# Kernel tuning notes

Hardware: AMD Instinct MI355X
Metric: run time of the kernel (lower is better)

## Reference

```python
import jax, jax.numpy as jnp
import numpy as np

EPS = 1e-5
HEADS = 8


def _bn(x, p):
    # p: [4, C] rows = (gamma, beta, running_mean, running_var); channel axis = 1 (eval-mode BN)
    shape = (1, p.shape[1]) + (1,) * (x.ndim - 2)
    g = p[0].reshape(shape); b = p[1].reshape(shape)
    m = p[2].reshape(shape); v = p[3].reshape(shape)
    return (x - m) * (g / jnp.sqrt(v + EPS)) + b


def _conv1x1(x, w):
    # x: [N, Cin, H, W], w: [Cout, Cin]
    return jnp.einsum('oc,nchw->nohw', w, x)


def _axial(x, kqv_w, kqv_bn, logits_bn, rel_enc, ks, height_dim):
    # x: [B, C, H, W]
    if height_dim:
        x = jnp.transpose(x, (0, 3, 1, 2))  # [B, W, C, H] -> attend over H (=ks)
    else:
        x = jnp.transpose(x, (0, 2, 1, 3))  # [B, H, C, W] -> attend over W (=ks)
    b, w, d, h = x.shape
    dh = d // HEADS
    xf = x.reshape(b * w, d, h)
    kqv = jnp.einsum('oc,ncl->nol', kqv_w, xf)          # conv1d k=1, [n, 2d, h]
    kqv = _bn(kqv, kqv_bn)
    kqv = kqv.reshape(b * w, HEADS, dh * 2, h)
    k = kqv[:, :, : dh // 2]                            # [n, H, dh/2, h]
    q = kqv[:, :, dh // 2: dh]                          # [n, H, dh/2, h]
    v = kqv[:, :, dh:]                                  # [n, H, dh,   h]
    # relative position encodings
    idx = jnp.arange(ks)[None, :] - jnp.arange(ks)[:, None] + ks - 1  # [ks, ks]
    rel = rel_enc[:, idx.reshape(-1)].reshape(dh * 2, ks, ks)
    q_enc = rel[: dh // 2]
    k_enc = rel[dh // 2: dh]
    v_enc = rel[dh:]
    qk = jnp.einsum('nhdx,nhdy->nhxy', q, k)
    qr = jnp.einsum('nhdx,dxy->nhxy', q, q_enc)
    kr = jnp.einsum('nhdx,dxy->nhyx', k, k_enc)         # einsum + transpose(2,3)
    logits = jnp.concatenate([qk, qr, kr], axis=1)       # [n, 3*H, h, h]
    logits = _bn(logits, logits_bn)
    logits = logits.reshape(b * w, 3, HEADS, h, h).sum(axis=1)
    weights = jax.nn.softmax(logits, axis=3)             # [n, H, h, h]
    attn = jnp.einsum('nhxy,nhdy->nhdx', weights, v)
    attn_enc = jnp.einsum('nhxy,dxy->nhdx', weights, v_enc)
    # cat along last dim + reshape + sum(dim=-2) in torch == elementwise sum here
    out = (attn + attn_enc).reshape(b, w, d, h)
    if height_dim:
        out = jnp.transpose(out, (0, 2, 3, 1))  # [B, C, H, W]
    else:
        out = jnp.transpose(out, (0, 2, 1, 3))  # [B, C, H, W]
    return out


def setup_inputs() -> dict:
    key = jax.random.key(0)
    ks = jax.random.split(key, 13)
    def rn(k, shape, s=0.05):
        return jax.random.normal(k, shape, jnp.float32) * s
    def rp(k, shape):
        return jax.random.uniform(k, shape, jnp.float32, minval=0.1, maxval=1.0)
    return {
        'x': jax.random.normal(ks[0], (1, 64, 256, 128), jnp.float32),
        'conv1_w': rn(ks[1], (64, 64)),
        'bn1': rp(ks[2], (4, 64)),
        'kqv_w_h': rn(ks[3], (128, 64)),
        'kqv_bn_h': rp(ks[4], (4, 128)),
        'logits_bn_h': rp(ks[5], (4, 24)),
        'rel_enc_h': rn(ks[6], (16, 511)),
        'kqv_w_w': rn(ks[7], (128, 64)),
        'kqv_bn_w': rp(ks[8], (4, 128)),
        'logits_bn_w': rp(ks[9], (4, 24)),
        'rel_enc_w': rn(ks[10], (16, 255)),
        'conv3_w': rn(ks[11], (64, 64)),
        'bn3': rp(ks[12], (4, 64)),
    }


def reference(x, conv1_w, bn1, kqv_w_h, kqv_bn_h, logits_bn_h, rel_enc_h,
              kqv_w_w, kqv_bn_w, logits_bn_w, rel_enc_w, conv3_w, bn3):
    out = jax.nn.relu(_bn(_conv1x1(x, conv1_w), bn1))
    out = _axial(out, kqv_w_h, kqv_bn_h, logits_bn_h, rel_enc_h, 256, True)
    out = _axial(out, kqv_w_w, kqv_bn_w, logits_bn_w, rel_enc_w, 128, False)
    out = jax.nn.relu(out)
    out = _bn(_conv1x1(out, conv3_w), bn3)
    return jax.nn.relu(out + x)
```

## Files before the change

### kernel.cpp

```cpp
#include <hip/hip_runtime.h>
#include <stdint.h>

#define EPSF 1e-5f
#define LOG2E 1.4426950408889634f

__device__ __forceinline__ float bflo(uint32_t u){ union{uint32_t u;float f;}c; c.u=u<<16; return c.f; }
__device__ __forceinline__ float bfhi(uint32_t u){ union{uint32_t u;float f;}c; c.u=u&0xffff0000u; return c.f; }
__device__ __forceinline__ float bfhiraw(uint32_t u){ union{uint32_t u;float f;}c; c.u=u; return c.f; }
__device__ __forceinline__ uint32_t f2bf(float f){ union{float f;uint32_t u;}c; c.f=f; uint32_t u=c.u; return (u + 0x7fffu + ((u>>16)&1u)) >> 16; }
__device__ __forceinline__ uint32_t pk2(float a, float b){ return f2bf(a) | (f2bf(b)<<16); }

__global__ void k_relpack(const float* __restrict__ relH, const float* __restrict__ relW,
                          uint4* __restrict__ rqkH, uint4* __restrict__ rveH,
                          uint4* __restrict__ rqkW, uint4* __restrict__ rveW) {
  int NJ = blockIdx.x ? 255 : 511;
  const float* rel = blockIdx.x ? relW : relH;
  uint4* rqk = blockIdx.x ? rqkW : rqkH;
  uint4* rve = blockIdx.x ? rveW : rveH;
  int j = threadIdx.x;
  if (j >= NJ) return;
  const float* q = rel;
  const float* k = rel + 4*NJ;
  const float* v = rel + 8*NJ;
  int jr = NJ-1-j;
  uint4 a;
  a.x = pk2(q[0*NJ+j], q[1*NJ+j]);
  a.y = pk2(q[2*NJ+j], q[3*NJ+j]);
  a.z = pk2(k[0*NJ+jr], k[1*NJ+jr]);
  a.w = pk2(k[2*NJ+jr], k[3*NJ+jr]);
  rqk[j] = a;
  uint4 b;
  b.x = pk2(v[0*NJ+j], v[1*NJ+j]);
  b.y = pk2(v[2*NJ+j], v[3*NJ+j]);
  b.z = pk2(v[4*NJ+j], v[5*NJ+j]);
  b.w = pk2(v[6*NJ+j], v[7*NJ+j]);
  rve[j] = b;
}

__global__ __launch_bounds__(256)
void k_conv1(const float* __restrict__ in, const float* __restrict__ w,
             const float* __restrict__ bn, float* __restrict__ out) {
  __shared__ float L[64*65];
  int tid = threadIdx.x;
  int p0 = blockIdx.x * 64;
  int lane = tid & 63;
  int wvs = __builtin_amdgcn_readfirstlane(tid >> 6);
  #pragma unroll
  for (int rr = 0; rr < 16; ++rr) {
    int c = wvs*16 + rr;
    L[c*64 + lane] = in[(size_t)c*32768 + p0 + lane];
  }
  __syncthreads();
  float xv[64];
  #pragma unroll
  for (int c = 0; c < 64; ++c) xv[c] = L[c*64 + lane];
  float val[16];
  #pragma unroll
  for (int r = 0; r < 16; ++r) {
    int o = wvs*16 + r;
    const float* wr = w + o*64;
    float acc = 0.f;
    #pragma unroll
    for (int c = 0; c < 64; ++c) acc = fmaf(wr[c], xv[c], acc);
    float s = bn[o] * rsqrtf(bn[192+o] + EPSF);
    val[r] = fmaxf(fmaf(acc, s, fmaf(-bn[128+o], s, bn[64+o])), 0.f);
  }
  __syncthreads();
  #pragma unroll
  for (int r = 0; r < 16; ++r) L[lane*65 + wvs*16 + r] = val[r];
  __syncthreads();
  float4* dst = (float4*)(out + (size_t)p0*64);
  #pragma unroll
  for (int k = 0; k < 4; ++k) {
    int f4 = tid + k*256;
    int f = f4*4; int p = f >> 6, o = f & 63;
    float4 v;
    v.x = L[p*65+o]; v.y = L[p*65+o+1]; v.z = L[p*65+o+2]; v.w = L[p*65+o+3];
    dst[f4] = v;
  }
}

template<int LEN, int RS, int CS>
__global__ __launch_bounds__(512)
void k_kqv(const float* __restrict__ in, const float* __restrict__ w,
           const float* __restrict__ bn, uint4* __restrict__ kvV,
           uint2* __restrict__ kvK, float* __restrict__ qb) {
  __shared__ float L[64*65];
  int tid = threadIdx.x;
  int n = blockIdx.x;
  int y0 = blockIdx.y * 64;
  #pragma unroll
  for (int rr = 0; rr < 8; ++rr) {
    int idx = tid + rr*512;
    int yy = idx >> 6, c = idx & 63;
    L[yy*65 + c] = in[((size_t)(y0+yy)*RS + (size_t)n*CS)*64 + c];
  }
  __syncthreads();
  int hd = __builtin_amdgcn_readfirstlane(tid >> 6);
  int yy = tid & 63;
  float xv[64];
  #pragma unroll
  for (int c = 0; c < 64; ++c) xv[c] = L[yy*65 + c];
  float val[16];
  #pragma unroll
  for (int r = 0; r < 16; ++r) {
    int o = hd*16 + r;
    const float* wr = w + o*64;
    float acc = 0.f;
    #pragma unroll
    for (int c = 0; c < 64; ++c) acc = fmaf(wr[c], xv[c], acc);
    float s = bn[o] * rsqrtf(bn[384+o] + EPSF);
    val[r] = fmaf(acc, s, fmaf(-bn[256+o], s, bn[128+o]));
  }
  size_t base = ((size_t)n*8 + hd)*LEN + (y0 + yy);
  kvK[base] = make_uint2(pk2(val[0],val[1]), pk2(val[2],val[3]));
  kvV[base] = make_uint4(pk2(val[8],val[9]),  pk2(val[10],val[11]),
                         pk2(val[12],val[13]), pk2(val[14],val[15]));
  float4 qq; qq.x = val[4]; qq.y = val[5]; qq.z = val[6]; qq.w = val[7];
  *(float4*)(qb + base*4) = qq;
}

template<int LEN, int G, bool RELUO, int XS, int NS>
__global__ __launch_bounds__(LEN*G/2, 2)
void k_attn2(const uint4* __restrict__ kvV, const uint2* __restrict__ kvK,
             const float* __restrict__ qb, const uint4* __restrict__ rqk,
             const uint4* __restrict__ rve, const float* __restrict__ lbn,
             float* __restrict__ out) {
  constexpr int NJ = 2*LEN-1;
  constexpr int HALF = LEN/2;
  constexpr int T = LEN*G/2;
  constexpr int YR = LEN/G;
  constexpr int CH = 4;
  constexpr size_t S1 = (size_t)LEN*48 + (size_t)NJ*48;
  constexpr size_t S2 = (size_t)(G-1)*LEN*40;
  constexpr size_t PS = S1 > S2 ? S1 : S2;
  int n  = blockIdx.x >> 3;
  int hd = blockIdx.x & 7;
  int t  = threadIdx.x;

  __shared__ __align__(16) char pool[PS];
  float4* sK   = (float4*)(pool);
  float4* sVa  = (float4*)(pool + (size_t)LEN*16);
  float4* sVb  = (float4*)(pool + (size_t)LEN*32);
  uint4*  sT   = (uint4*) (pool + (size_t)LEN*48);
  float4* sVE0 = (float4*)(pool + (size_t)LEN*48 + (size_t)NJ*16);
  float4* sVE1 = (float4*)(pool + (size_t)LEN*48 + (size_t)NJ*32);

  size_t kvbase = ((size_t)n*8 + hd)*LEN;
  for (int i = t; i < LEN; i += T) {
    uint2 kk = kvK[kvbase + i];
    uint4 vv = kvV[kvbase + i];
    sK[i]  = make_float4(bflo(kk.x), bfhi(kk.x), bflo(kk.y), bfhi(kk.y));
    sVa[i] = make_float4(bflo(vv.x), bfhi(vv.x), bflo(vv.y), bfhi(vv.y));
    sVb[i] = make_float4(bflo(vv.z), bfhi(vv.z), bflo(vv.w), bfhi(vv.w));
  }
  for (int j = t; j < NJ; j += T) {
    sT[j] = rqk[j];
    uint4 ve = rve[j];
    sVE0[j] = make_float4(bflo(ve.x), bfhi(ve.x), bflo(ve.y), bfhi(ve.y));
    sVE1[j] = make_float4(bflo(ve.z), bfhi(ve.z), bflo(ve.w), bfhi(ve.w));
  }

  float A0,A1,A2,Bc;
  {
    int c0 = hd, c1 = 8+hd, c2 = 16+hd;
    float s0 = lbn[c0]*rsqrtf(lbn[72+c0]+EPSF);
    float s1 = lbn[c1]*rsqrtf(lbn[72+c1]+EPSF);
    float s2 = lbn[c2]*rsqrtf(lbn[72+c2]+EPSF);
    float t0 = fmaf(-lbn[48+c0], s0, lbn[24+c0]);
    float t1 = fmaf(-lbn[48+c1], s1, lbn[24+c1]);
    float t2 = fmaf(-lbn[48+c2], s2, lbn[24+c2]);
    A0 = s0*LOG2E; A1 = s1*LOG2E; A2 = s2*LOG2E; Bc = (t0+t1+t2)*LOG2E;
  }

  int g  = t / HALF;
  int tl = t % HALF;
  int y0 = g * YR;

  float q[2][4];
  #pragma unroll
  for (int i = 0; i < 2; ++i) {
    float4 qq = *(const float4*)(qb + (kvbase + tl + i*HALF)*4);
    q[i][0]=qq.x; q[i][1]=qq.y; q[i][2]=qq.z; q[i][3]=qq.w;
  }
  float m[2], ss[2], acc[2][8], lr[2][CH];
  #pragma unroll
  for (int i=0;i<2;++i){ m[i]=-3.0e38f; ss[i]=0.f;
    #pragma unroll
    for(int d=0;d<8;++d) acc[i][d]=0.f; }

  __syncthreads();

  for (int yc = 0; yc < YR; yc += CH) {
    #pragma unroll
    for (int c = 0; c < CH; ++c) {
      int y = y0 + yc + c;
      float4 kk = sK[y];
      #pragma unroll
      for (int i = 0; i < 2; ++i) {
        int j = y - (tl + i*HALF) + (LEN-1);
        uint4 qe = sT[j];
        float qk = fmaf(q[i][3],kk.w, fmaf(q[i][2],kk.z, fmaf(q[i][1],kk.y, q[i][0]*kk.x)));
        float qr = fmaf(q[i][1],bfhiraw(qe.x), q[i][0]*bflo(qe.x));
        qr = fmaf(q[i][3],bfhiraw(qe.y), fmaf(q[i][2],bflo(qe.y), qr));
        float kr = fmaf(kk.y,bfhiraw(qe.z), kk.x*bflo(qe.z));
        kr = fmaf(kk.w,bfhiraw(qe.w), fmaf(kk.z,bflo(qe.w), kr));
        lr[i][c] = fmaf(qk,A0, fmaf(qr,A1, fmaf(kr,A2, Bc)));
      }
    }
    #pragma unroll
    for (int i = 0; i < 2; ++i) {
      float cm = fmaxf(fmaxf(lr[i][0], lr[i][1]), fmaxf(lr[i][2], lr[i][3]));
      float mn = fmaxf(m[i], cm);
      float sc = __builtin_amdgcn_exp2f(m[i] - mn);
      m[i] = mn; ss[i] *= sc;
      #pragma unroll
      for (int d = 0; d < 8; ++d) acc[i][d] *= sc;
    }
    #pragma unroll
    for (int c = 0; c < CH; ++c) {
      int y = y0 + yc + c;
      float4 va = sVa[y], vb = sVb[y];
      #pragma unroll
      for (int i = 0; i < 2; ++i) {
        int j = y - (tl + i*HALF) + (LEN-1);
        float4 ea = sVE0[j];
        float4 eb = sVE1[j];
        float e = __builtin_amdgcn_exp2f(lr[i][c] - m[i]);
        ss[i] += e;
        acc[i][0] = fmaf(e, va.x + ea.x, acc[i][0]);
        acc[i][1] = fmaf(e, va.y + ea.y, acc[i][1]);
        acc[i][2] = fmaf(e, va.z + ea.z, acc[i][2]);
        acc[i][3] = fmaf(e, va.w + ea.w, acc[i][3]);
        acc[i][4] = fmaf(e, vb.x + eb.x, acc[i][4]);
        acc[i][5] = fmaf(e, vb.y + eb.y, acc[i][5]);
        acc[i][6] = fmaf(e, vb.z + eb.z, acc[i][6]);
        acc[i][7] = fmaf(e, vb.w + eb.w, acc[i][7]);
      }
    }
  }

  __syncthreads();
  float4* M0 = (float4*)(pool);
  float4* M1 = (float4*)(pool + (size_t)(G-1)*LEN*16);
  float2* MS = (float2*)(pool + (size_t)(G-1)*LEN*32);
  if (g > 0) {
    #pragma unroll
    for (int i = 0; i < 2; ++i) {
      int slot = ((g-1)*HALF + tl)*2 + i;
      M0[slot] = make_float4(acc[i][0],acc[i][1],acc[i][2],acc[i][3]);
      M1[slot] = make_float4(acc[i][4],acc[i][5],acc[i][6],acc[i][7]);
      MS[slot] = make_float2(m[i], ss[i]);
    }
  }
  __syncthreads();
  if (g == 0) {
    #pragma unroll
    for (int i = 0; i < 2; ++i) {
      float M = m[i];
      float2 oms[G-1];
      #pragma unroll
      for (int gg = 1; gg < G; ++gg) {
        oms[gg-1] = MS[((gg-1)*HALF + tl)*2 + i];
        M = fmaxf(M, oms[gg-1].x);
      }
      float w0 = __builtin_amdgcn_exp2f(m[i] - M);
      float st = ss[i]*w0;
      float a[8];
      #pragma unroll
      for (int d = 0; d < 8; ++d) a[d] = acc[i][d]*w0;
      #pragma unroll
      for (int gg = 1; gg < G; ++gg) {
        int slot = ((gg-1)*HALF + tl)*2 + i;
        float wg = __builtin_amdgcn_exp2f(oms[gg-1].x - M);
        st += oms[gg-1].y*wg;
        float4 a0 = M0[slot];
        float4 a1 = M1[slot];
        a[0] = fmaf(a0.x, wg, a[0]); a[1] = fmaf(a0.y, wg, a[1]);
        a[2] = fmaf(a0.z, wg, a[2]); a[3] = fmaf(a0.w, wg, a[3]);
        a[4] = fmaf(a1.x, wg, a[4]); a[5] = fmaf(a1.y, wg, a[5]);
        a[6] = fmaf(a1.z, wg, a[6]); a[7] = fmaf(a1.w, wg, a[7]);
      }
      float inv = 1.0f / st;
      int x = tl + i*HALF;
      float* dst = out + ((size_t)x*XS + (size_t)n*NS)*64 + hd*8;
      float4 lo, hi;
      lo.x = a[0]*inv; lo.y = a[1]*inv; lo.z = a[2]*inv; lo.w = a[3]*inv;
      hi.x = a[4]*inv; hi.y = a[5]*inv; hi.z = a[6]*inv; hi.w = a[7]*inv;
      if (RELUO) {
        lo.x=fmaxf(lo.x,0.f); lo.y=fmaxf(lo.y,0.f); lo.z=fmaxf(lo.z,0.f); lo.w=fmaxf(lo.w,0.f);
        hi.x=fmaxf(hi.x,0.f); hi.y=fmaxf(hi.y,0.f); hi.z=fmaxf(hi.z,0.f); hi.w=fmaxf(hi.w,0.f);
      }
      *(float4*)dst = lo;
      *((float4*)dst + 1) = hi;
    }
  }
}

__global__ __launch_bounds__(256)
void k_conv3(const float* __restrict__ in, const float* __restrict__ w,
             const float* __restrict__ bn, const float* __restrict__ resid,
             float* __restrict__ out) {
  __shared__ float L[64*65];
  int tid = threadIdx.x;
  int p0 = blockIdx.x * 64;
  const float4* src = (const float4*)(in + (size_t)p0*64);
  #pragma unroll
  for (int k = 0; k < 4; ++k) {
    int f4 = tid + k*256;
    float4 v = src[f4];
    int f = f4*4; int p = f >> 6, o = f & 63;
    L[p*65+o] = v.x; L[p*65+o+1] = v.y; L[p*65+o+2] = v.z; L[p*65+o+3] = v.w;
  }
  __syncthreads();
  int lane = tid & 63;
  int wvs = __builtin_amdgcn_readfirstlane(tid >> 6);
  float xv[64];
  #pragma unroll
  for (int c = 0; c < 64; ++c) xv[c] = L[lane*65 + c];
  #pragma unroll
  for (int r = 0; r < 16; ++r) {
    int o = wvs*16 + r;
    const float* wr = w + o*64;
    float acc = 0.f;
    #pragma unroll
    for (int c = 0; c < 64; ++c) acc = fmaf(wr[c], xv[c], acc);
    float s = bn[o] * rsqrtf(bn[192+o] + EPSF);
    float val = fmaf(acc, s, fmaf(-bn[128+o], s, bn[64+o]));
    size_t idx = (size_t)o*32768 + p0 + lane;
    out[idx] = fmaxf(val + resid[idx], 0.f);
  }
}

extern "C" void kernel_launch(void* const* d_in, const int* in_sizes, int n_in,
                              void* d_out, int out_size, void* d_ws, size_t ws_size,
                              hipStream_t stream) {
  const float* x         = (const float*)d_in[0];
  const float* conv1_w   = (const float*)d_in[1];
  const float* bn1       = (const float*)d_in[2];
  const float* kqv_w_h   = (const float*)d_in[3];
  const float* kqv_bn_h  = (const float*)d_in[4];
  const float* lbn_h     = (const float*)d_in[5];
  const float* rel_h     = (const float*)d_in[6];
  const float* kqv_w_w   = (const float*)d_in[7];
  const float* kqv_bn_w  = (const float*)d_in[8];
  const float* lbn_w     = (const float*)d_in[9];
  const float* rel_w     = (const float*)d_in[10];
  const float* conv3_w   = (const float*)d_in[11];
  const float* bn3       = (const float*)d_in[12];
  float* outp = (float*)d_out;
  char* ws = (char*)d_ws;

  float* A    = (float*)(ws);
  uint4* kvV  = (uint4*)(ws + 8388608);
  uint2* kvK  = (uint2*)(ws + 12582912);
  float* qb   = (float*)(ws + 14680064);
  uint4* rqkH = (uint4*)(ws + 18874368);
  uint4* rveH = (uint4*)(ws + 18882560);
  uint4* rqkW = (uint4*)(ws + 18890752);
  uint4* rveW = (uint4*)(ws + 18894848);

  k_relpack<<<2, 512, 0, stream>>>(rel_h, rel_w, rqkH, rveH, rqkW, rveW);

  k_conv1<<<512, 256, 0, stream>>>(x, conv1_w, bn1, A);

  k_kqv<256,128,1><<<dim3(128,4), 512, 0, stream>>>(A, kqv_w_h, kqv_bn_h, kvV, kvK, qb);
  k_attn2<256,4,false,128,1><<<1024, 512, 0, stream>>>(kvV, kvK, qb, rqkH, rveH, lbn_h, A);

  k_kqv<128,1,128><<<dim3(256,2), 512, 0, stream>>>(A, kqv_w_w, kqv_bn_w, kvV, kvK, qb);
  k_attn2<128,4,true,1,128><<<2048, 256, 0, stream>>>(kvV, kvK, qb, rqkW, rveW, lbn_w, A);

  k_conv3<<<512, 256, 0, stream>>>(A, conv3_w, bn3, x, outp);
}
```

Baseline: 189.9 us.

## Use packed fp32 FMA and fold logit BN scales into K and rel-encodings

Rewrites the 1x1 conv dot products (conv1, kqv, conv3) and the attention inner loops with 2-wide float vectors so the compiler can emit packed fp32 FMAs. In the attention kernel, the per-head logit BN scales are folded into pre-scaled K and relative-encoding tables in LDS, stored as fp32, and the constant BN bias is dropped because softmax is invariant to it. conv1's LDS staging is transposed to match the new access pattern. This cuts VALU instruction count in the hot loops, at the cost of more LDS per attention block and a changed summation order.

```diff
diff --git a/kernel.cpp b/kernel.cpp
--- a/kernel.cpp
+++ b/kernel.cpp
@@ -3,6 +3,9 @@
 
 #define EPSF 1e-5f
 #define LOG2E 1.4426950408889634f
+
+typedef float f32x2 __attribute__((ext_vector_type(2)));
+typedef float f32x4 __attribute__((ext_vector_type(4)));
 
 __device__ __forceinline__ float bflo(uint32_t u){ union{uint32_t u;float f;}c; c.u=u<<16; return c.f; }
 __device__ __forceinline__ float bfhi(uint32_t u){ union{uint32_t u;float f;}c; c.u=u&0xffff0000u; return c.f; }
@@ -48,20 +51,24 @@
   #pragma unroll
   for (int rr = 0; rr < 16; ++rr) {
     int c = wvs*16 + rr;
-    L[c*64 + lane] = in[(size_t)c*32768 + p0 + lane];
-  }
-  __syncthreads();
-  float xv[64];
-  #pragma unroll
-  for (int c = 0; c < 64; ++c) xv[c] = L[c*64 + lane];
+    L[lane*65 + c] = in[(size_t)c*32768 + p0 + lane];
+  }
+  __syncthreads();
+  f32x2 xv2[32];
+  #pragma unroll
+  for (int c2 = 0; c2 < 32; ++c2) {
+    xv2[c2].x = L[lane*65 + 2*c2];
+    xv2[c2].y = L[lane*65 + 2*c2 + 1];
+  }
   float val[16];
   #pragma unroll
   for (int r = 0; r < 16; ++r) {
     int o = wvs*16 + r;
-    const float* wr = w + o*64;
-    float acc = 0.f;
-    #pragma unroll
-    for (int c = 0; c < 64; ++c) acc = fmaf(wr[c], xv[c], acc);
+    const f32x2* wr = (const f32x2*)(w + o*64);
+    f32x2 a2 = {0.f, 0.f};
+    #pragma unroll
+    for (int c2 = 0; c2 < 32; ++c2) a2 = wr[c2]*xv2[c2] + a2;
+    float acc = a2.x + a2.y;
     float s = bn[o] * rsqrtf(bn[192+o] + EPSF);
     val[r] = fmaxf(fmaf(acc, s, fmaf(-bn[128+o], s, bn[64+o])), 0.f);
   }
@@ -98,17 +105,21 @@
   __syncthreads();
   int hd = __builtin_amdgcn_readfirstlane(tid >> 6);
   int yy = tid & 63;
-  float xv[64];
-  #pragma unroll
-  for (int c = 0; c < 64; ++c) xv[c] = L[yy*65 + c];
+  f32x2 xv2[32];
+  #pragma unroll
+  for (int c2 = 0; c2 < 32; ++c2) {
+    xv2[c2].x = L[yy*65 + 2*c2];
+    xv2[c2].y = L[yy*65 + 2*c2 + 1];
+  }
   float val[16];
   #pragma unroll
   for (int r = 0; r < 16; ++r) {
     int o = hd*16 + r;
-    const float* wr = w + o*64;
-    float acc = 0.f;
-    #pragma unroll
-    for (int c = 0; c < 64; ++c) acc = fmaf(wr[c], xv[c], acc);
+    const f32x2* wr = (const f32x2*)(w + o*64);
+    f32x2 a2 = {0.f, 0.f};
+    #pragma unroll
+    for (int c2 = 0; c2 < 32; ++c2) a2 = wr[c2]*xv2[c2] + a2;
+    float acc = a2.x + a2.y;
     float s = bn[o] * rsqrtf(bn[384+o] + EPSF);
     val[r] = fmaf(acc, s, fmaf(-bn[256+o], s, bn[128+o]));
   }
@@ -131,7 +142,7 @@
   constexpr int T = LEN*G/2;
   constexpr int YR = LEN/G;
   constexpr int CH = 4;
-  constexpr size_t S1 = (size_t)LEN*48 + (size_t)NJ*48;
+  constexpr size_t S1 = (size_t)LEN*64 + (size_t)NJ*48;
   constexpr size_t S2 = (size_t)(G-1)*LEN*40;
   constexpr size_t PS = S1 > S2 ? S1 : S2;
   int n  = blockIdx.x >> 3;
@@ -139,55 +150,59 @@
   int t  = threadIdx.x;
 
   __shared__ __align__(16) char pool[PS];
-  float4* sK   = (float4*)(pool);
-  float4* sVa  = (float4*)(pool + (size_t)LEN*16);
-  float4* sVb  = (float4*)(pool + (size_t)LEN*32);
-  uint4*  sT   = (uint4*) (pool + (size_t)LEN*48);
-  float4* sVE0 = (float4*)(pool + (size_t)LEN*48 + (size_t)NJ*16);
-  float4* sVE1 = (float4*)(pool + (size_t)LEN*48 + (size_t)NJ*32);
+  f32x4* sKt = (f32x4*)(pool);
+  f32x4* sKr = (f32x4*)(pool + (size_t)LEN*16);
+  f32x4* sVa = (f32x4*)(pool + (size_t)LEN*32);
+  f32x4* sVb = (f32x4*)(pool + (size_t)LEN*48);
+  f32x4* sQE = (f32x4*)(pool + (size_t)LEN*64);
+  f32x4* sKE = (f32x4*)(pool + (size_t)LEN*64 + (size_t)NJ*16);
+  uint4* sVE = (uint4*)(pool + (size_t)LEN*64 + (size_t)NJ*32);
+
+  float A0L, A1L, A2L;
+  {
+    int c0 = hd, c1 = 8+hd, c2 = 16+hd;
+    A0L = lbn[c0]*rsqrtf(lbn[72+c0]+EPSF)*LOG2E;
+    A1L = lbn[c1]*rsqrtf(lbn[72+c1]+EPSF)*LOG2E;
+    A2L = lbn[c2]*rsqrtf(lbn[72+c2]+EPSF)*LOG2E;
+  }
 
   size_t kvbase = ((size_t)n*8 + hd)*LEN;
   for (int i = t; i < LEN; i += T) {
     uint2 kk = kvK[kvbase + i];
     uint4 vv = kvV[kvbase + i];
-    sK[i]  = make_float4(bflo(kk.x), bfhi(kk.x), bflo(kk.y), bfhi(kk.y));
-    sVa[i] = make_float4(bflo(vv.x), bfhi(vv.x), bflo(vv.y), bfhi(vv.y));
-    sVb[i] = make_float4(bflo(vv.z), bfhi(vv.z), bflo(vv.w), bfhi(vv.w));
+    float k0=bflo(kk.x), k1=bfhi(kk.x), k2=bflo(kk.y), k3=bfhi(kk.y);
+    f32x4 kt; kt.x=k0*A0L; kt.y=k1*A0L; kt.z=k2*A0L; kt.w=k3*A0L;
+    sKt[i] = kt;
+    f32x4 kr; kr.x=k0; kr.y=k1; kr.z=k2; kr.w=k3;
+    sKr[i] = kr;
+    f32x4 va; va.x=bflo(vv.x); va.y=bfhi(vv.x); va.z=bflo(vv.y); va.w=bfhi(vv.y);
+    sVa[i] = va;
+    f32x4 vb; vb.x=bflo(vv.z); vb.y=bfhi(vv.z); vb.z=bflo(vv.w); vb.w=bfhi(vv.w);
+    sVb[i] = vb;
   }
   for (int j = t; j < NJ; j += T) {
-    sT[j] = rqk[j];
-    uint4 ve = rve[j];
-    sVE0[j] = make_float4(bflo(ve.x), bfhi(ve.x), bflo(ve.y), bfhi(ve.y));
-    sVE1[j] = make_float4(bflo(ve.z), bfhi(ve.z), bflo(ve.w), bfhi(ve.w));
-  }
-
-  float A0,A1,A2,Bc;
-  {
-    int c0 = hd, c1 = 8+hd, c2 = 16+hd;
-    float s0 = lbn[c0]*rsqrtf(lbn[72+c0]+EPSF);
-    float s1 = lbn[c1]*rsqrtf(lbn[72+c1]+EPSF);
-    float s2 = lbn[c2]*rsqrtf(lbn[72+c2]+EPSF);
-    float t0 = fmaf(-lbn[48+c0], s0, lbn[24+c0]);
-    float t1 = fmaf(-lbn[48+c1], s1, lbn[24+c1]);
-    float t2 = fmaf(-lbn[48+c2], s2, lbn[24+c2]);
-    A0 = s0*LOG2E; A1 = s1*LOG2E; A2 = s2*LOG2E; Bc = (t0+t1+t2)*LOG2E;
+    uint4 a = rqk[j];
+    f32x4 qe; qe.x=bflo(a.x)*A1L; qe.y=bfhi(a.x)*A1L; qe.z=bflo(a.y)*A1L; qe.w=bfhi(a.y)*A1L;
+    sQE[j] = qe;
+    f32x4 ke; ke.x=bflo(a.z)*A2L; ke.y=bfhi(a.z)*A2L; ke.z=bflo(a.w)*A2L; ke.w=bfhi(a.w)*A2L;
+    sKE[j] = ke;
+    sVE[j] = rve[j];
   }
 
   int g  = t / HALF;
   int tl = t % HALF;
   int y0 = g * YR;
 
-  float q[2][4];
-  #pragma unroll
-  for (int i = 0; i < 2; ++i) {
-    float4 qq = *(const float4*)(qb + (kvbase + tl + i*HALF)*4);
-    q[i][0]=qq.x; q[i][1]=qq.y; q[i][2]=qq.z; q[i][3]=qq.w;
-  }
-  float m[2], ss[2], acc[2][8], lr[2][CH];
+  f32x4 qv[2];
+  qv[0] = *(const f32x4*)(qb + (kvbase + tl)*4);
+  qv[1] = *(const f32x4*)(qb + (kvbase + tl + HALF)*4);
+
+  float m[2], ss[2], lr[2][CH];
+  f32x2 acc2[2][4];
   #pragma unroll
   for (int i=0;i<2;++i){ m[i]=-3.0e38f; ss[i]=0.f;
     #pragma unroll
-    for(int d=0;d<8;++d) acc[i][d]=0.f; }
+    for(int d=0;d<4;++d){ acc2[i][d].x=0.f; acc2[i][d].y=0.f; } }
 
   __syncthreads();
 
@@ -195,17 +210,19 @@
     #pragma unroll
     for (int c = 0; c < CH; ++c) {
       int y = y0 + yc + c;
-      float4 kk = sK[y];
+      f32x4 kt = sKt[y];
+      f32x4 kr = sKr[y];
       #pragma unroll
       for (int i = 0; i < 2; ++i) {
         int j = y - (tl + i*HALF) + (LEN-1);
-        uint4 qe = sT[j];
-        float qk = fmaf(q[i][3],kk.w, fmaf(q[i][2],kk.z, fmaf(q[i][1],kk.y, q[i][0]*kk.x)));
-        float qr = fmaf(q[i][1],bfhiraw(qe.x), q[i][0]*bflo(qe.x));
-        qr = fmaf(q[i][3],bfhiraw(qe.y), fmaf(q[i][2],bflo(qe.y), qr));
-        float kr = fmaf(kk.y,bfhiraw(qe.z), kk.x*bflo(qe.z));
-        kr = fmaf(kk.w,bfhiraw(qe.w), fmaf(kk.z,bflo(qe.w), kr));
-        lr[i][c] = fmaf(qk,A0, fmaf(qr,A1, fmaf(kr,A2, Bc)));
+        f32x4 qe = sQE[j];
+        f32x4 ke = sKE[j];
+        f32x2 t0 = kt.lo + qe.lo;
+        f32x2 t1 = kt.hi + qe.hi;
+        f32x2 s = qv[i].lo*t0 + qv[i].hi*t1;
+        s = kr.lo*ke.lo + s;
+        s = kr.hi*ke.hi + s;
+        lr[i][c] = s.x + s.y;
       }
     }
     #pragma unroll
@@ -214,28 +231,29 @@
       float mn = fmaxf(m[i], cm);
       float sc = __builtin_amdgcn_exp2f(m[i] - mn);
       m[i] = mn; ss[i] *= sc;
-      #pragma unroll
-      for (int d = 0; d < 8; ++d) acc[i][d] *= sc;
+      f32x2 sc2 = {sc, sc};
+      #pragma unroll
+      for (int d = 0; d < 4; ++d) acc2[i][d] *= sc2;
     }
     #pragma unroll
     for (int c = 0; c < CH; ++c) {
       int y = y0 + yc + c;
-      float4 va = sVa[y], vb = sVb[y];
+      f32x4 va = sVa[y], vb = sVb[y];
       #pragma unroll
       for (int i = 0; i < 2; ++i) {
         int j = y - (tl + i*HALF) + (LEN-1);
-        float4 ea = sVE0[j];
-        float4 eb = sVE1[j];
+        uint4 ve = sVE[j];
         float e = __builtin_amdgcn_exp2f(lr[i][c] - m[i]);
         ss[i] += e;
-        acc[i][0] = fmaf(e, va.x + ea.x, acc[i][0]);
-        acc[i][1] = fmaf(e, va.y + ea.y, acc[i][1]);
-        acc[i][2] = fmaf(e, va.z + ea.z, acc[i][2]);
-        acc[i][3] = fmaf(e, va.w + ea.w, acc[i][3]);
-        acc[i][4] = fmaf(e, vb.x + eb.x, acc[i][4]);
-        acc[i][5] = fmaf(e, vb.y + eb.y, acc[i][5]);
-        acc[i][6] = fmaf(e, vb.z + eb.z, acc[i][6]);
-        acc[i][7] = fmaf(e, vb.w + eb.w, acc[i][7]);
+        f32x2 e2 = {e, e};
+        f32x2 w0; w0.x = bflo(ve.x); w0.y = bfhiraw(ve.x); w0 = va.lo + w0;
+        f32x2 w1; w1.x = bflo(ve.y); w1.y = bfhiraw(ve.y); w1 = va.hi + w1;
+        f32x2 w2; w2.x = bflo(ve.z); w2.y = bfhiraw(ve.z); w2 = vb.lo + w2;
+        f32x2 w3; w3.x = bflo(ve.w); w3.y = bfhiraw(ve.w); w3 = vb.hi + w3;
+        acc2[i][0] = e2*w0 + acc2[i][0];
+        acc2[i][1] = e2*w1 + acc2[i][1];
+        acc2[i][2] = e2*w2 + acc2[i][2];
+        acc2[i][3] = e2*w3 + acc2[i][3];
       }
     }
   }
@@ -248,8 +266,8 @@
     #pragma unroll
     for (int i = 0; i < 2; ++i) {
       int slot = ((g-1)*HALF + tl)*2 + i;
-      M0[slot] = make_float4(acc[i][0],acc[i][1],acc[i][2],acc[i][3]);
-      M1[slot] = make_float4(acc[i][4],acc[i][5],acc[i][6],acc[i][7]);
+      M0[slot] = make_float4(acc2[i][0].x,acc2[i][0].y,acc2[i][1].x,acc2[i][1].y);
+      M1[slot] = make_float4(acc2[i][2].x,acc2[i][2].y,acc2[i][3].x,acc2[i][3].y);
       MS[slot] = make_float2(m[i], ss[i]);
     }
   }
@@ -267,8 +285,8 @@
       float w0 = __builtin_amdgcn_exp2f(m[i] - M);
       float st = ss[i]*w0;
       float a[8];
-      #pragma unroll
-      for (int d = 0; d < 8; ++d) a[d] = acc[i][d]*w0;
+      a[0]=acc2[i][0].x*w0; a[1]=acc2[i][0].y*w0; a[2]=acc2[i][1].x*w0; a[3]=acc2[i][1].y*w0;
+      a[4]=acc2[i][2].x*w0; a[5]=acc2[i][2].y*w0; a[6]=acc2[i][3].x*w0; a[7]=acc2[i][3].y*w0;
       #pragma unroll
       for (int gg = 1; gg < G; ++gg) {
         int slot = ((gg-1)*HALF + tl)*2 + i;
@@ -315,16 +333,20 @@
   __syncthreads();
   int lane = tid & 63;
   int wvs = __builtin_amdgcn_readfirstlane(tid >> 6);
-  float xv[64];
-  #pragma unroll
-  for (int c = 0; c < 64; ++c) xv[c] = L[lane*65 + c];
+  f32x2 xv2[32];
+  #pragma unroll
+  for (int c2 = 0; c2 < 32; ++c2) {
+    xv2[c2].x = L[lane*65 + 2*c2];
+    xv2[c2].y = L[lane*65 + 2*c2 + 1];
+  }
   #pragma unroll
   for (int r = 0; r < 16; ++r) {
     int o = wvs*16 + r;
-    const float* wr = w + o*64;
-    float acc = 0.f;
-    #pragma unroll
-    for (int c = 0; c < 64; ++c) acc = fmaf(wr[c], xv[c], acc);
+    const f32x2* wr = (const f32x2*)(w + o*64);
+    f32x2 a2 = {0.f, 0.f};
+    #pragma unroll
+    for (int c2 = 0; c2 < 32; ++c2) a2 = wr[c2]*xv2[c2] + a2;
+    float acc = a2.x + a2.y;
     float s = bn[o] * rsqrtf(bn[192+o] + EPSF);
     float val = fmaf(acc, s, fmaf(-bn[128+o], s, bn[64+o]));
     size_t idx = (size_t)o*32768 + p0 + lane;
```

Result: no change. 187.0 us (-1.5%).
